# Optimization experiments

Measured on AMD Instinct MI355X. Metric: run time of the kernel, lower is better.

Reference implementation:

```python
import jax, jax.numpy as jnp
import numpy as np

NUM_QUERIES = 256
NUM_NEGATIVES = 512
NUM_GENERALIZED = 8
GEN_RADIUS = 1.0
TEMP = 0.5
STRONG_THRESHOLD = 0.97


def _mls(mu0, mu1, s0, s1):
    # mutual likelihood score; mu's are L2-normalized (F.normalize, eps=1e-12)
    mu0 = mu0 / jnp.maximum(jnp.linalg.norm(mu0, axis=-1, keepdims=True), 1e-12)
    mu1 = mu1 / jnp.maximum(jnp.linalg.norm(mu1, axis=-1, keepdims=True), 1e-12)
    down = s0 + s1
    return -0.5 * (((mu0 - mu1) ** 2) / down + jnp.log(down)).mean(-1)


def setup_inputs() -> dict:
    key = jax.random.key(0)
    B, S, H, W, C = 4, 19, 128, 128, 256
    ks = jax.random.split(key, 6)
    mu = jax.random.normal(ks[0], (B, C, H, W), jnp.float32)
    sigma = jax.random.uniform(ks[1], (B, C, H, W), jnp.float32, minval=0.1, maxval=1.0)
    cls = jax.random.randint(ks[2], (B, H, W), 0, S)
    label = jnp.transpose(jax.nn.one_hot(cls, S, dtype=jnp.float32), (0, 3, 1, 2))  # [B,S,H,W]
    mask = jnp.ones((B, 1, H, W), jnp.float32)
    prob = jax.random.uniform(ks[3], (B, S, H, W), jnp.float32)
    mmt_prototype_mu = jax.random.normal(ks[4], (S, 1, C), jnp.float32)
    mmt_prototype_sigma = jax.random.uniform(ks[5], (S, 1, C), jnp.float32, minval=0.1, maxval=1.0)
    return {"mu": mu, "sigma": sigma, "label": label, "mask": mask, "prob": prob,
            "mmt_prototype_mu": mmt_prototype_mu, "mmt_prototype_sigma": mmt_prototype_sigma,
            "epoch": 0, "iter_i": 0}


def reference(mu, sigma, label, mask, prob, mmt_prototype_mu, mmt_prototype_sigma, epoch, iter_i):
    B, C, H, W = mu.shape
    S = label.shape[1]
    P = B * H * W
    Q, NEG, G = NUM_QUERIES, NUM_NEGATIVES, NUM_GENERALIZED
    key = jax.random.key(1234)

    valid = (label * mask).transpose(1, 0, 2, 3).reshape(S, P)            # [S,P] float
    mu_f = mu.transpose(0, 2, 3, 1).reshape(P, C)                          # [P,C]
    sg_f = sigma.transpose(0, 2, 3, 1).reshape(P, C)
    prob_f = prob.transpose(1, 0, 2, 3).reshape(S, P)
    hard = (prob_f < STRONG_THRESHOLD).astype(valid.dtype) * valid         # [S,P]

    # --- segment prototypes (precision-weighted fusion), detached as in torch.no_grad ---
    inv_sg = 1.0 / sg_f
    proto_sigma_b = 1.0 / jnp.einsum('sp,pc->sc', valid, inv_sg)           # [S,C]
    proto_mu_b = proto_sigma_b * jnp.einsum('sp,pc->sc', valid, inv_sg * mu_f)
    mmt_mu = mmt_prototype_mu[:, 0, :]
    mmt_sg = mmt_prototype_sigma[:, 0, :]
    proto_sigma = 1.0 / (1.0 / proto_sigma_b + 1.0 / mmt_sg)               # momentum fusion
    proto_mu = proto_sigma * (mmt_mu / mmt_sg + proto_mu_b / proto_sigma_b)
    proto_mu = jax.lax.stop_gradient(proto_mu)
    proto_sigma = jax.lax.stop_gradient(proto_sigma)

    # cumulative masks for uniform sampling over valid / hard pixels via searchsorted
    valid_cum = jnp.cumsum(valid, axis=1)                                  # [S,P]
    valid_cnt = valid_cum[:, -1]
    hard_cum = jnp.cumsum(hard, axis=1)
    hard_cnt = hard_cum[:, -1]

    loss = jnp.float32(0.0)
    for i in range(S):
        ki = jax.random.fold_in(key, i)
        k_anc, k_cls, k_neg, k_gen = jax.random.split(ki, 4)
        # anchors: uniform over hard pixels of segment i
        u = jax.random.uniform(k_anc, (Q,)) * hard_cnt[i]
        a_idx = jnp.clip(jnp.searchsorted(hard_cum[i], u, side='right'), 0, P - 1)
        anchor_mu = mu_f[a_idx]                                            # [Q,C]
        anchor_sg = sg_f[a_idx]
        # negative class distribution from prototype MLS similarity
        others = jnp.concatenate([jnp.arange(i + 1, S), jnp.arange(0, i)])  # [S-1]
        sim = _mls(proto_mu[i][None], proto_mu[others], proto_sigma[i][None], proto_sigma[others])
        logp = jax.nn.log_softmax(sim / TEMP)
        samp = jax.random.categorical(k_cls, logp, shape=(Q, NEG))          # idx into `others`
        cls_g = others[samp.reshape(-1)]                                    # [Q*NEG] global class
        # uniform pixel within each sampled class (vectorized searchsorted over classes)
        un = jax.random.uniform(k_neg, (Q * NEG,))
        idx_all = jax.vmap(lambda cs, cnt: jnp.searchsorted(cs, un * cnt, side='right'))(valid_cum, valid_cnt)
        n_idx = jnp.clip(idx_all[cls_g, jnp.arange(Q * NEG)], 0, P - 1)
        neg_mu = jax.lax.stop_gradient(mu_f[n_idx].reshape(Q, NEG, C))
        neg_sg = jax.lax.stop_gradient(sg_f[n_idx].reshape(Q, NEG, C))
        pos_mu = jnp.broadcast_to(proto_mu[i][None, None], (Q, 1, C))
        pos_sg = jnp.broadcast_to(proto_sigma[i][None, None], (Q, 1, C))
        # generalized negatives: reparameterized samples from (updated) momentum prototypes
        eps = jax.random.normal(k_gen, (S - 1, G, C))
        gen = proto_mu[others][:, None, :] + GEN_RADIUS * jnp.sqrt(proto_sigma[others])[:, None, :] * eps
        gen = jnp.broadcast_to(gen.reshape(1, (S - 1) * G, C), (Q, (S - 1) * G, C))
        all_mu = jnp.concatenate([pos_mu, neg_mu, gen], axis=1)             # [Q,1+NEG+(S-1)*G,C]
        all_sg = jnp.concatenate([pos_sg, neg_sg, jnp.zeros_like(gen)], axis=1)
        logits = _mls(anchor_mu[:, None, :], all_mu, anchor_sg[:, None, :], all_sg) / TEMP
        loss = loss - jax.nn.log_softmax(logits, axis=-1)[:, 0].mean()      # CE vs target 0
    return loss / S
```

## Files before the change

kernel.cpp:

```cpp
#include <hip/hip_runtime.h>
#include <hip/hip_fp16.h>
#include <hip/hip_fp8.h>
#include <cstdint>

#define B_   4
#define S_   19
#define HW_  16384
#define P_   65536
#define C_   256
#define Q_   256
#define NEG_ 512
#define NS_  131072
#define GENV_ 144
#define NANCH (S_ * 256)
#define NPAIR (NANCH / 2)
#define NBUCK 8

typedef float v2f __attribute__((ext_vector_type(2)));

#if __has_builtin(__builtin_amdgcn_cvt_pk_f32_fp8) && __has_builtin(__builtin_amdgcn_cvt_pk_fp8_f32)
#define HAVE_HW_FP8 1
#endif

template<int W> __device__ __forceinline__ v2f cvt8(uint32_t d) {
#ifdef HAVE_HW_FP8
  v2f r = __builtin_amdgcn_cvt_pk_f32_fp8((int)d, W);
  return r;
#else
  __hip_fp8_e4m3 h0, h1;
  h0.__x = (uint8_t)(d >> (W * 16));
  h1.__x = (uint8_t)(d >> (W * 16 + 8));
  v2f r; r.x = (float)h0; r.y = (float)h1; return r;
#endif
}
template<int W> __device__ __forceinline__ uint32_t pk8(float a, float b, uint32_t old) {
#ifdef HAVE_HW_FP8
  return (uint32_t)__builtin_amdgcn_cvt_pk_fp8_f32(a, b, (int)old, W);
#else
  __hip_fp8_e4m3 ha(a), hb(b);
  uint32_t v = (uint32_t)ha.__x | ((uint32_t)hb.__x << 8);
  return (old & (W ? 0x0000FFFFu : 0xFFFF0000u)) | (v << (W * 16));
#endif
}

__device__ __forceinline__ void tf2x32(uint32_t k0, uint32_t k1, uint32_t x0, uint32_t x1,
                                       uint32_t& o0, uint32_t& o1) {
  uint32_t k2 = k0 ^ k1 ^ 0x1BD11BDAu;
#define TFR(r) { x0 += x1; x1 = (x1 << r) | (x1 >> (32 - r)); x1 ^= x0; }
  x0 += k0; x1 += k1;
  TFR(13) TFR(15) TFR(26) TFR(6)  x0 += k1; x1 += k2 + 1u;
  TFR(17) TFR(29) TFR(16) TFR(24) x0 += k2; x1 += k0 + 2u;
  TFR(13) TFR(15) TFR(26) TFR(6)  x0 += k0; x1 += k1 + 3u;
  TFR(17) TFR(29) TFR(16) TFR(24) x0 += k1; x1 += k2 + 4u;
  TFR(13) TFR(15) TFR(26) TFR(6)  x0 += k2; x1 += k0 + 5u;
#undef TFR
  o0 = x0; o1 = x1;
}

__device__ __forceinline__ uint32_t rbits(uint32_t k0, uint32_t k1, uint32_t n) {
  uint32_t a, b; tf2x32(k0, k1, 0u, n, a, b); return a ^ b;
}

__device__ __forceinline__ float bits2f01(uint32_t b) {
  return __uint_as_float((b >> 9) | 0x3f800000u) - 1.0f;
}

__device__ __forceinline__ float fastrcp(float x) {
  float r; asm("v_rcp_f32 %0, %1" : "=v"(r) : "v"(x)); return r;
}

__device__ __forceinline__ float wred(float v) {
#pragma unroll
  for (int off = 32; off > 0; off >>= 1) v += __shfl_xor(v, off, 64);
  return v;
}
__device__ __forceinline__ void wred3(float& a, float& b, float& c) {
#pragma unroll
  for (int off = 32; off > 0; off >>= 1) {
    a += __shfl_xor(a, off, 64);
    b += __shfl_xor(b, off, 64);
    c += __shfl_xor(c, off, 64);
  }
}

__device__ __forceinline__ void lse_up(float lg, float& m, float& l) {
  if (lg > m) { l = l * __expf(m - lg) + 1.0f; m = lg; }
  else l += __expf(lg - m);
}
__device__ __forceinline__ void lse_merge(float& m, float& l, float mo, float lo) {
  float mn = fmaxf(m, mo);
  l = l * __expf(m - mn) + lo * __expf(mo - mn);
  m = mn;
}

__device__ __forceinline__ float erfinv_f(float x) {
  float w = -__logf(fmaxf(fmaf(-x, x, 1.0f), 1e-37f));
  float p;
  if (w < 5.0f) {
    w -= 2.5f;
    p = 2.81022636e-08f;
    p = fmaf(p, w, 3.43273939e-07f);
    p = fmaf(p, w, -3.5233877e-06f);
    p = fmaf(p, w, -4.39150654e-06f);
    p = fmaf(p, w, 0.00021858087f);
    p = fmaf(p, w, -0.00125372503f);
    p = fmaf(p, w, -0.00417768164f);
    p = fmaf(p, w, 0.246640727f);
    p = fmaf(p, w, 1.50140941f);
  } else {
    w = sqrtf(w) - 3.0f;
    p = -0.000200214257f;
    p = fmaf(p, w, 0.000100950558f);
    p = fmaf(p, w, 0.00134934322f);
    p = fmaf(p, w, -0.00367342844f);
    p = fmaf(p, w, 0.00573950773f);
    p = fmaf(p, w, -0.0076224613f);
    p = fmaf(p, w, 0.00943887047f);
    p = fmaf(p, w, 1.00167406f);
    p = fmaf(p, w, 2.83297682f);
  }
  return p * x;
}

__global__ __launch_bounds__(256) void k_classify(const float* __restrict__ label,
    const float* __restrict__ mask, const float* __restrict__ prob,
    uint32_t* __restrict__ keys, int* __restrict__ cls, int* __restrict__ hrd,
    int* __restrict__ bcv, int* __restrict__ bch) {
  __shared__ int hv[S_], hh[S_];
  int t = threadIdx.x;
  if (t < S_) { hv[t] = 0; hh[t] = 0; }
  if (blockIdx.x == 0 && t < S_) {
    uint32_t f0, f1;
    tf2x32(0u, 1234u, 0u, (uint32_t)t, f0, f1);
#pragma unroll
    for (int k = 0; k < 4; ++k) {
      uint32_t a, b;
      tf2x32(f0, f1, 0u, (uint32_t)k, a, b);
      keys[t * 8 + k * 2] = a; keys[t * 8 + k * 2 + 1] = b;
    }
  }
  __syncthreads();
  int p = blockIdx.x * 256 + t;
  int b = p >> 14, rem = p & (HW_ - 1);
  int sp = -1;
#pragma unroll
  for (int s = 0; s < S_; ++s) {
    float l = label[((b * S_ + s) << 14) + rem];
    if (l > 0.5f) sp = s;
  }
  if (mask[(b << 14) + rem] <= 0.5f) sp = -1;
  int h = 0;
  if (sp >= 0) h = (prob[((b * S_ + sp) << 14) + rem] < 0.97f) ? 1 : 0;
  cls[p] = sp; hrd[p] = h;
  if (sp >= 0) { atomicAdd(&hv[sp], 1); if (h) atomicAdd(&hh[sp], 1); }
  __syncthreads();
  if (t < S_) { bcv[t * 256 + blockIdx.x] = hv[t]; bch[t * 256 + blockIdx.x] = hh[t]; }
}

__global__ __launch_bounds__(256) void k_norm(const float* __restrict__ mu,
    float2* __restrict__ rnrm) {
  int p = blockIdx.x * 256 + threadIdx.x;
  int b = p >> 14, rem = p & (HW_ - 1);
  const float* base = mu + (((size_t)(b * C_)) << 14) + rem;
  float s2 = 0.f;
#pragma unroll 4
  for (int c = 0; c < C_; ++c) {
    float v = base[(size_t)c << 14];
    s2 = fmaf(v, v, s2);
  }
  float nrm = sqrtf(s2);
  rnrm[p] = make_float2(fastrcp(fmaxf(nrm, 1e-12f)), nrm);
}

__global__ __launch_bounds__(256) void k_pack(const float* __restrict__ mu,
    const float* __restrict__ sg, const float2* __restrict__ rnrm,
    uint32_t* __restrict__ pair8) {
  __shared__ float smu[64][65];
  __shared__ float ssg[64][65];
  __shared__ float srn[64];
  int p0 = blockIdx.x * 64, c0 = blockIdx.y * 64;
  int b = p0 >> 14, rem0 = p0 & (HW_ - 1);
  if (threadIdx.x < 64) srn[threadIdx.x] = rnrm[p0 + threadIdx.x].x;
  int px = threadIdx.x & 63, cy = threadIdx.x >> 6;
#pragma unroll
  for (int itr = 0; itr < 16; ++itr) {
    int cl = cy + itr * 4;
    int addr = ((b * C_ + c0 + cl) << 14) + rem0 + px;
    smu[cl][px] = mu[addr];
    ssg[cl][px] = sg[addr];
  }
  __syncthreads();
#pragma unroll
  for (int itr = 0; itr < 8; ++itr) {
    int e = itr * 256 + threadIdx.x;
    int pxl = e >> 5, dw = e & 31, cl = dw * 2;
    float rn = srn[pxl];
    uint32_t wd = pk8<0>(smu[cl][pxl] * rn, ssg[cl][pxl], 0u);
    wd = pk8<1>(smu[cl + 1][pxl] * rn, ssg[cl + 1][pxl], wd);
    pair8[(size_t)(p0 + pxl) * 128 + (c0 >> 1) + dw] = wd;
  }
}

__global__ __launch_bounds__(320) void k_scan(const int* __restrict__ bcv, const int* __restrict__ bch,
    int* __restrict__ bov, int* __restrict__ boh,
    int* __restrict__ cntv, int* __restrict__ cnth,
    int* __restrict__ basev, int* __restrict__ baseh) {
  __shared__ int psv[S_][16], psh[S_][16], scv[S_], sch[S_];
  int t = threadIdx.x;
  int s = t >> 4, c = t & 15;
  if (t < 304) {
    int sv = 0, sh = 0;
#pragma unroll 4
    for (int b = 0; b < 16; ++b) {
      sv += bcv[s * 256 + c * 16 + b];
      sh += bch[s * 256 + c * 16 + b];
    }
    psv[s][c] = sv; psh[s][c] = sh;
  }
  __syncthreads();
  if (t < S_) {
    int rv = 0, rh = 0;
#pragma unroll
    for (int cc = 0; cc < 16; ++cc) {
      int tv = psv[t][cc]; psv[t][cc] = rv; rv += tv;
      int th = psh[t][cc]; psh[t][cc] = rh; rh += th;
    }
    cntv[t] = rv; cnth[t] = rh; scv[t] = rv; sch[t] = rh;
  }
  __syncthreads();
  if (t == 0) {
    int bv = 0, bh = 0;
    for (int k = 0; k < S_; ++k) { basev[k] = bv; bv += scv[k]; baseh[k] = bh; bh += sch[k]; }
  }
  if (t < 304) {
    int rv = psv[s][c], rh = psh[s][c];
#pragma unroll 4
    for (int b = 0; b < 16; ++b) {
      int i0 = s * 256 + c * 16 + b;
      int tv = bcv[i0]; bov[i0] = rv; rv += tv;
      int th = bch[i0]; boh[i0] = rh; rh += th;
    }
  }
}

__global__ __launch_bounds__(256) void k_fill(const int* __restrict__ cls, const int* __restrict__ hrd,
    const int* __restrict__ bov, const int* __restrict__ boh,
    const int* __restrict__ basev, const int* __restrict__ baseh,
    int* __restrict__ posv, int* __restrict__ posh) {
  __shared__ int lc[256], lh[256];
  int t = threadIdx.x;
  int p = blockIdx.x * 256 + t;
  int s = cls[p]; int h = hrd[p];
  lc[t] = s; lh[t] = h;
  __syncthreads();
  if (s >= 0) {
    int rv = 0, rh = 0;
    for (int k = 0; k < t; ++k) { if (lc[k] == s) { rv++; rh += lh[k]; } }
    posv[basev[s] + bov[s * 256 + blockIdx.x] + rv] = p;
    if (h) posh[baseh[s] + boh[s * 256 + blockIdx.x] + rh] = p;
  }
}

__global__ __launch_bounds__(256) void k_sums(const uint32_t* __restrict__ pair8,
    const float2* __restrict__ rnrm, const int* __restrict__ cls, float* __restrict__ part) {
  __shared__ float lacc[S_][2][C_];
  __shared__ int scls[256];
  __shared__ float snrm[256];
  int t = threadIdx.x;
  for (int e = t; e < S_ * 2 * C_; e += 256) (&lacc[0][0][0])[e] = 0.f;
  int p0 = blockIdx.x * 256;
  scls[t] = cls[p0 + t];
  snrm[t] = rnrm[p0 + t].y;
  __syncthreads();
  int half = t & 1, dwi = t >> 1;
  uint32_t d = pair8[(size_t)p0 * 128 + dwi];
  for (int pp = 0; pp < 256; ++pp) {
    uint32_t dnx = (pp + 1 < 256) ? pair8[(size_t)(p0 + pp + 1) * 128 + dwi] : 0u;
    int s = scls[pp];
    if (s >= 0) {
      v2f e = half ? cvt8<1>(d) : cvt8<0>(d);
      float ia = fastrcp(e.y);
      lacc[s][0][t] += ia;
      lacc[s][1][t] += ia * e.x * snrm[pp];
    }
    d = dnx;
  }
  __syncthreads();
  float* dst = part + (size_t)blockIdx.x * (2 * S_ * C_);
  for (int e = t; e < S_ * 2 * C_; e += 256) dst[e] = (&lacc[0][0][0])[e];
}

__global__ __launch_bounds__(256) void k_proto(const float* __restrict__ part,
    const float* __restrict__ mmu, const float* __restrict__ msg,
    float* __restrict__ pmu, float* __restrict__ psig, float* __restrict__ phat) {
  int s = blockIdx.x, c = threadIdx.x;
  float A = 0.f, Bv = 0.f;
  for (int b = 0; b < 256; ++b) {
    const float* pb = part + (size_t)b * (2 * S_ * C_) + (s * 2) * C_;
    A += pb[c];
    Bv += pb[C_ + c];
  }
  int e = s * C_ + c;
  float psb = 1.0f / A;
  float pmb = psb * Bv;
  float ms = msg[e], mm = mmu[e];
  float ps = 1.0f / (1.0f / psb + 1.0f / ms);
  float pm = ps * (mm / ms + pmb / psb);
  pmu[e] = pm; psig[e] = ps;
  __shared__ float red[4];
  float w = wred(pm * pm);
  int lane = c & 63, wv = c >> 6;
  if (lane == 0) red[wv] = w;
  __syncthreads();
  float tot = red[0] + red[1] + red[2] + red[3];
  float nrm = fmaxf(sqrtf(tot), 1e-12f);
  phat[e] = pm / nrm;
}

__global__ __launch_bounds__(64) void k_simlogp(const float* __restrict__ phat,
    const float* __restrict__ psig, float* __restrict__ logp) {
  int i = blockIdx.x, lane = threadIdx.x;
  int c0 = lane * 4;
  float phi[4], psi[4];
#pragma unroll
  for (int k = 0; k < 4; ++k) { phi[k] = phat[i * C_ + c0 + k]; psi[k] = psig[i * C_ + c0 + k]; }
  float xs[18];
#pragma unroll
  for (int j = 0; j < 18; ++j) {
    int o = i + 1 + j; if (o >= S_) o -= S_;
    float t = 0.f;
#pragma unroll
    for (int k = 0; k < 4; ++k) {
      float d = phi[k] - phat[o * C_ + c0 + k];
      float dn = psi[k] + psig[o * C_ + c0 + k];
      t += d * d / dn + logf(dn);
    }
    t = wred(t);
    xs[j] = (-0.5f * t * (1.0f / 256.0f)) * 2.0f;
  }
  float m = xs[0];
#pragma unroll
  for (int j = 1; j < 18; ++j) m = fmaxf(m, xs[j]);
  float se = 0.f;
#pragma unroll
  for (int j = 0; j < 18; ++j) se += expf(xs[j] - m);
  float lg = logf(se);
  if (lane == 0) {
#pragma unroll
    for (int j = 0; j < 18; ++j) logp[i * 18 + j] = xs[j] - m - lg;
  }
}

__global__ __launch_bounds__(256) void k_gen(const uint32_t* __restrict__ keys,
    const float* __restrict__ pmu, const float* __restrict__ psig, float* __restrict__ ghat) {
  int v = blockIdx.x, i = blockIdx.y, c = threadIdx.x;
  int o = i + 1 + (v >> 3); if (o >= S_) o -= S_;
  uint32_t k0 = keys[i * 8 + 6], k1 = keys[i * 8 + 7];
  uint32_t bits = rbits(k0, k1, (uint32_t)(v * C_ + c));
  float f01 = bits2f01(bits);
  const float lo = -0.99999994f;
  float u = fmaxf(f01 * 2.0f + lo, lo);
  float eps = 1.41421356237f * erfinv_f(u);
  float g = pmu[o * C_ + c] + sqrtf(psig[o * C_ + c]) * eps;
  __shared__ float red[4];
  float w = wred(g * g);
  int lane = c & 63, wv = c >> 6;
  if (lane == 0) red[wv] = w;
  __syncthreads();
  float tot = red[0] + red[1] + red[2] + red[3];
  float nrm = fmaxf(sqrtf(tot), 1e-12f);
  ghat[((size_t)(i * GENV_ + v)) * C_ + c] = g / nrm;
}

__global__ __launch_bounds__(256) void k_sample(const uint32_t* __restrict__ keys,
    const float* __restrict__ logp, const int* __restrict__ cntv, const int* __restrict__ basev,
    const int* __restrict__ posv, int* __restrict__ nidx) {
  int i = blockIdx.y;
  int m = blockIdx.x * 256 + threadIdx.x;
  __shared__ float elp[18];
  __shared__ int lcnt[S_], lbase[S_];
  int t = threadIdx.x;
  if (t < 18) elp[t] = __expf(-logp[i * 18 + t]);
  if (t < S_) { lcnt[t] = cntv[t]; lbase[t] = basev[t]; }
  __syncthreads();
  uint32_t kc0 = keys[i * 8 + 2], kc1 = keys[i * 8 + 3];
  uint32_t kn0 = keys[i * 8 + 4], kn1 = keys[i * 8 + 5];
  float bv = 1e30f; int best = 0;
  for (int s = 0; s < 18; ++s) {
    uint32_t b = rbits(kc0, kc1, (uint32_t)m * 18u + (uint32_t)s);
    float u = fmaxf(bits2f01(b), 1.17549435e-38f);
    float val = (-__logf(u)) * elp[s];
    if (val < bv) { bv = val; best = s; }
  }
  float un = bits2f01(rbits(kn0, kn1, (uint32_t)m));
  int cc = i + 1 + best; if (cc >= S_) cc -= S_;
  int cnt = lcnt[cc];
  int idx = P_ - 1;
  if (cnt > 0) {
    int kk = (int)(un * (float)cnt);
    if (kk >= cnt) kk = cnt - 1;
    idx = posv[lbase[cc] + kk];
  }
  nidx[(size_t)i * NS_ + m] = idx;
}

__global__ __launch_bounds__(64) void k_bucket(const uint32_t* __restrict__ keys,
    const int* __restrict__ cnth, const int* __restrict__ baseh, const int* __restrict__ posh,
    const int* __restrict__ nidx, int* __restrict__ snidx, int* __restrict__ boff,
    int* __restrict__ aidx) {
  int a = blockIdx.x;
  int lane = threadIdx.x;
  if (lane == 0) {
    int i = a >> 8, q = a & 255;
    uint32_t k0 = keys[i * 8 + 0], k1 = keys[i * 8 + 1];
    float u = bits2f01(rbits(k0, k1, (uint32_t)q));
    int cnt = cnth[i];
    int idx = P_ - 1;
    if (cnt > 0) {
      int kk = (int)(u * (float)cnt);
      if (kk >= cnt) kk = cnt - 1;
      idx = posh[baseh[i] + kk];
    }
    aidx[a] = idx;
  }
  const int* src = nidx + (size_t)a * NEG_;
  int e[8], bk[8];
#pragma unroll
  for (int c = 0; c < 8; ++c) { e[c] = src[c * 64 + lane]; bk[c] = (e[c] >> 13) & 7; }
  uint32_t cnt[NBUCK];
#pragma unroll
  for (int b = 0; b < NBUCK; ++b) cnt[b] = 0;
#pragma unroll
  for (int c = 0; c < 8; ++c)
#pragma unroll
    for (int b = 0; b < NBUCK; ++b) {
      unsigned long long mb = __ballot(bk[c] == b);
      cnt[b] += (uint32_t)__popcll(mb);
    }
  uint32_t base[NBUCK]; uint32_t run = 0;
#pragma unroll
  for (int b = 0; b < NBUCK; ++b) { base[b] = run; run += cnt[b]; }
  if (lane < NBUCK) boff[a * 9 + lane] = (int)base[lane];
  if (lane == 0) boff[a * 9 + 8] = NEG_;
  uint32_t off[NBUCK];
#pragma unroll
  for (int b = 0; b < NBUCK; ++b) off[b] = 0;
  unsigned long long ltm = (1ull << lane) - 1ull;
#pragma unroll
  for (int c = 0; c < 8; ++c) {
    int pos = 0;
#pragma unroll
    for (int b = 0; b < NBUCK; ++b) {
      unsigned long long mb = __ballot(bk[c] == b);
      if (bk[c] == b) pos = (int)(base[b] + off[b] + (uint32_t)__popcll(mb & ltm));
      off[b] += (uint32_t)__popcll(mb);
    }
    snidx[(size_t)a * NEG_ + pos] = e[c];
  }
}

__global__ __launch_bounds__(64) void k_neg(const uint32_t* __restrict__ pair8,
    const int* __restrict__ snidx, const int* __restrict__ boff,
    const int* __restrict__ aidx, float2* __restrict__ partial) {
  __shared__ float4 anc[260];
  int bid = blockIdx.x;
  int bucket = bid & 7;
  int pr = bid >> 3;
  int a0 = pr * 2, a1 = a0 + 1;
  int lane = threadIdx.x;

  int ap0 = aidx[a0], ap1 = aidx[a1];
  uint2 d0 = ((const uint2*)(pair8 + (size_t)ap0 * 128))[lane];
  uint2 d1 = ((const uint2*)(pair8 + (size_t)ap1 * 128))[lane];
  {
    v2f ex = cvt8<0>(d0.x), ey = cvt8<1>(d0.x), ez = cvt8<0>(d0.y), ew = cvt8<1>(d0.y);
    anc[lane * 2]     = make_float4(ex.x, ex.y, ey.x, ey.y);
    anc[lane * 2 + 1] = make_float4(ez.x, ez.y, ew.x, ew.y);
    ex = cvt8<0>(d1.x); ey = cvt8<1>(d1.x); ez = cvt8<0>(d1.y); ew = cvt8<1>(d1.y);
    anc[130 + lane * 2]     = make_float4(ex.x, ex.y, ey.x, ey.y);
    anc[130 + lane * 2 + 1] = make_float4(ez.x, ez.y, ew.x, ew.y);
  }
  __syncthreads();

  int s0 = boff[a0 * 9 + bucket], e0i = boff[a0 * 9 + bucket + 1];
  int s1 = boff[a1 * 9 + bucket], e1i = boff[a1 * 9 + bucket + 1];
  int L0 = e0i - s0, L1 = e1i - s1, Lt = L0 + L1;
  const int* list0 = snidx + (size_t)a0 * NEG_ + s0;
  const int* list1 = snidx + (size_t)a1 * NEG_ + s1;

  float m0 = -1e30f, l0 = 0.f, m1 = -1e30f, l1 = 0.f;

  for (int r = 0; r * 64 < Lt; ++r) {
    int g = r * 64 + lane;
    bool act = g < Lt;
    int which = (act && g >= L0) ? 1 : 0;
    int j = which ? (g - L0) : g;
    int p = act ? (which ? list1[j] : list0[j]) : ap0;
    const uint4* rp = (const uint4*)(pair8 + (size_t)p * 128);
    const float4* A = anc + which * 130;
    float sT = 0.f, sL = 0.f;
    uint4 c0 = rp[0], c1 = rp[1];
#pragma unroll 1
    for (int it = 0; it < 16; ++it) {
      int nx = ((it + 1) & 15) * 2;
      uint4 n0 = rp[nx], n1 = rp[nx + 1];
      uint32_t dws[8] = {c0.x, c0.y, c0.z, c0.w, c1.x, c1.y, c1.z, c1.w};
      float pp = 1.0f, pq = 1.0f;
#pragma unroll
      for (int gq = 0; gq < 4; ++gq) {
        float4 acA = A[it * 8 + gq * 2];
        float4 acB = A[it * 8 + gq * 2 + 1];
        v2f e0v = cvt8<0>(dws[2 * gq]),     e1v = cvt8<1>(dws[2 * gq]);
        v2f e2v = cvt8<0>(dws[2 * gq + 1]), e3v = cvt8<1>(dws[2 * gq + 1]);
        float dn0 = acA.y + e0v.y, dn1 = acA.w + e1v.y;
        float dn2 = acB.y + e2v.y, dn3 = acB.w + e3v.y;
        float d01 = dn0 * dn1, d23 = dn2 * dn3;
        float R01 = fastrcp(d01), R23 = fastrcp(d23);
        pp *= d01; pq *= d23;
        float r0 = dn1 * R01, r1 = dn0 * R01, r2 = dn3 * R23, r3 = dn2 * R23;
        float f0 = acA.x - e0v.x, f1 = acA.z - e1v.x;
        float f2 = acB.x - e2v.x, f3 = acB.z - e3v.x;
        sT = fmaf(f0 * f0, r0, sT); sT = fmaf(f1 * f1, r1, sT);
        sT = fmaf(f2 * f2, r2, sT); sT = fmaf(f3 * f3, r3, sT);
      }
      sL += __logf(pp * pq);
      c0 = n0; c1 = n1;
    }
    float lg = -(sT + sL) * (1.0f / 256.0f);
    if (act) { if (which) lse_up(lg, m1, l1); else lse_up(lg, m0, l0); }
  }
#pragma unroll
  for (int o = 32; o > 0; o >>= 1) {
    float mo = __shfl_xor(m0, o, 64), lo = __shfl_xor(l0, o, 64);
    lse_merge(m0, l0, mo, lo);
    mo = __shfl_xor(m1, o, 64); lo = __shfl_xor(l1, o, 64);
    lse_merge(m1, l1, mo, lo);
  }
  if (lane == 0) {
    partial[a0 * NBUCK + bucket] = make_float2(m0, l0);
    partial[a1 * NBUCK + bucket] = make_float2(m1, l1);
  }
}

__global__ __launch_bounds__(256, 4) void k_fin(const uint32_t* __restrict__ pair8,
    const float* __restrict__ phat, const float* __restrict__ psig,
    const float* __restrict__ ghat, const int* __restrict__ aidx,
    const float2* __restrict__ partial, float* __restrict__ out) {
  __shared__ float2 ancG[C_];
  __shared__ float redm[3][4];
  __shared__ float2 mlw[4];

  int bid = blockIdx.x;
  int i = bid >> 8;
  int t = threadIdx.x, w = t >> 6, lane = t & 63;

  int ap = aidx[bid];
  uint32_t ad = pair8[(size_t)ap * 128 + (t >> 1)];
  v2f ae0 = cvt8<0>(ad), ae1 = cvt8<1>(ad);
  float ahat = (t & 1) ? ae1.x : ae0.x;
  float asg = (t & 1) ? ae1.y : ae0.y;
  float wv = fastrcp(asg);
  ancG[t] = make_float2(wv, ahat * wv);

  float pm = phat[i * C_ + t];
  float ps = psig[i * C_ + t];
  float dnp = asg + ps;
  float dd = ahat - pm;
  float post = fmaf(dd * dd, fastrcp(dnp), __logf(dnp));
  float a1t = ahat * ahat * wv;
  float lat = __logf(asg);
  wred3(post, a1t, lat);
  if (lane == 0) { redm[0][w] = post; redm[1][w] = a1t; redm[2][w] = lat; }
  __syncthreads();
  float postS = redm[0][0] + redm[0][1] + redm[0][2] + redm[0][3];
  float Kc = (redm[1][0] + redm[1][1] + redm[1][2] + redm[1][3])
           + (redm[2][0] + redm[2][1] + redm[2][2] + redm[2][3]);
  float logit0 = -postS * (1.0f / 256.0f);

  float m = -1e30f, l = 0.0f;
  const float4* ancGf = (const float4*)ancG;
  if (lane < 36) {
    int g = lane * 4 + w;
    const float4* gp = (const float4*)(ghat + ((size_t)(i * GENV_ + g)) * C_);
    float a1 = 0.f, a2 = 0.f;
    for (int itr = 0; itr < 64; ++itr) {
      float4 gv = gp[itr];
      float4 g01 = ancGf[itr * 2];
      float4 g23 = ancGf[itr * 2 + 1];
      a1 = fmaf(gv.x * gv.x, g01.x, a1); a2 = fmaf(gv.x, g01.y, a2);
      a1 = fmaf(gv.y * gv.y, g01.z, a1); a2 = fmaf(gv.y, g01.w, a2);
      a1 = fmaf(gv.z * gv.z, g23.x, a1); a2 = fmaf(gv.z, g23.y, a2);
      a1 = fmaf(gv.w * gv.w, g23.z, a1); a2 = fmaf(gv.w, g23.w, a2);
    }
    float lg = -(Kc + a1 - 2.0f * a2) * (1.0f / 256.0f);
    lse_up(lg, m, l);
  }
#pragma unroll
  for (int o = 32; o > 0; o >>= 1) {
    float mo = __shfl_xor(m, o, 64);
    float lo = __shfl_xor(l, o, 64);
    lse_merge(m, l, mo, lo);
  }
  if (lane == 0) mlw[w] = make_float2(m, l);
  __syncthreads();
  if (t == 0) {
    float mm = mlw[0].x, ll = mlw[0].y;
    lse_merge(mm, ll, mlw[1].x, mlw[1].y);
    lse_merge(mm, ll, mlw[2].x, mlw[2].y);
    lse_merge(mm, ll, mlw[3].x, mlw[3].y);
    const float2* pp = partial + (size_t)bid * NBUCK;
#pragma unroll
    for (int b = 0; b < NBUCK; ++b) lse_merge(mm, ll, pp[b].x, pp[b].y);
    lse_merge(mm, ll, logit0, 1.0f);
    float lse = mm + __logf(ll);
    float contrib = logit0 - lse;
    atomicAdd(out, -contrib * (1.0f / (19.0f * 256.0f)));
  }
}

extern "C" void kernel_launch(void* const* d_in, const int* in_sizes, int n_in,
                              void* d_out, int out_size, void* d_ws, size_t ws_size,
                              hipStream_t stream) {
  const float* mu    = (const float*)d_in[0];
  const float* sg    = (const float*)d_in[1];
  const float* label = (const float*)d_in[2];
  const float* mask  = (const float*)d_in[3];
  const float* prob  = (const float*)d_in[4];
  const float* mmu   = (const float*)d_in[5];
  const float* msg   = (const float*)d_in[6];

  char* ws = (char*)d_ws;
  size_t off = 0;
  auto take = [&](size_t bytes) { size_t r = off; off = (off + bytes + 255) & ~(size_t)255; return r; };
  size_t o_pair8 = take((size_t)P_ * 128 * 4);
  size_t o_rnrm  = take((size_t)P_ * 8);
  size_t o_cls   = take((size_t)P_ * 4);
  size_t o_hrd   = take((size_t)P_ * 4);
  size_t o_bcv   = take(S_ * 256 * 4);
  size_t o_bch   = take(S_ * 256 * 4);
  size_t o_bov   = take(S_ * 256 * 4);
  size_t o_boh   = take(S_ * 256 * 4);
  size_t o_cntv  = take(S_ * 4);
  size_t o_cnth  = take(S_ * 4);
  size_t o_basev = take(S_ * 4);
  size_t o_baseh = take(S_ * 4);
  size_t o_posv  = take((size_t)P_ * 4);
  size_t o_posh  = take((size_t)P_ * 4);
  size_t o_part  = take((size_t)256 * 2 * S_ * C_ * 4);
  size_t o_pmu   = take(S_ * C_ * 4);
  size_t o_psig  = take(S_ * C_ * 4);
  size_t o_phat  = take(S_ * C_ * 4);
  size_t o_logp  = take(S_ * 18 * 4);
  size_t o_keys  = take(S_ * 8 * 4);
  size_t o_aidx  = take(S_ * Q_ * 4);
  size_t o_nidx  = take((size_t)S_ * NS_ * 4);
  size_t o_snidx = take((size_t)S_ * NS_ * 4);
  size_t o_boff  = take((size_t)NANCH * 9 * 4);
  size_t o_lpar  = take((size_t)NANCH * NBUCK * 8);
  size_t o_ghat  = take((size_t)S_ * GENV_ * C_ * 4);
  if (ws_size < off) return;

  uint32_t* pair8 = (uint32_t*)(ws + o_pair8);
  float2*   rnrm  = (float2*)(ws + o_rnrm);
  int*      cls   = (int*)(ws + o_cls);
  int*      hrd   = (int*)(ws + o_hrd);
  int*      bcv   = (int*)(ws + o_bcv);
  int*      bch   = (int*)(ws + o_bch);
  int*      bov   = (int*)(ws + o_bov);
  int*      boh   = (int*)(ws + o_boh);
  int*      cntv  = (int*)(ws + o_cntv);
  int*      cnth  = (int*)(ws + o_cnth);
  int*      basev = (int*)(ws + o_basev);
  int*      baseh = (int*)(ws + o_baseh);
  int*      posv  = (int*)(ws + o_posv);
  int*      posh  = (int*)(ws + o_posh);
  float*    part  = (float*)(ws + o_part);
  float*    pmu   = (float*)(ws + o_pmu);
  float*    psig  = (float*)(ws + o_psig);
  float*    phat  = (float*)(ws + o_phat);
  float*    logp  = (float*)(ws + o_logp);
  uint32_t* keys  = (uint32_t*)(ws + o_keys);
  int*      aidx  = (int*)(ws + o_aidx);
  int*      nidx  = (int*)(ws + o_nidx);
  int*      snidx = (int*)(ws + o_snidx);
  int*      boff  = (int*)(ws + o_boff);
  float2*   lpar  = (float2*)(ws + o_lpar);
  float*    ghat  = (float*)(ws + o_ghat);

  hipMemsetAsync(d_out, 0, (size_t)out_size * 4, stream);

  k_classify<<<256, 256, 0, stream>>>(label, mask, prob, keys, cls, hrd, bcv, bch);
  k_norm<<<256, 256, 0, stream>>>(mu, rnrm);
  k_pack<<<dim3(P_ / 64, C_ / 64), 256, 0, stream>>>(mu, sg, rnrm, pair8);
  k_scan<<<1, 320, 0, stream>>>(bcv, bch, bov, boh, cntv, cnth, basev, baseh);
  k_fill<<<256, 256, 0, stream>>>(cls, hrd, bov, boh, basev, baseh, posv, posh);
  k_sums<<<256, 256, 0, stream>>>(pair8, rnrm, cls, part);
  k_proto<<<S_, 256, 0, stream>>>(part, mmu, msg, pmu, psig, phat);
  k_simlogp<<<S_, 64, 0, stream>>>(phat, psig, logp);
  k_gen<<<dim3(GENV_, S_), 256, 0, stream>>>(keys, pmu, psig, ghat);
  k_sample<<<dim3(512, S_), 256, 0, stream>>>(keys, logp, cntv, basev, posv, nidx);
  k_bucket<<<NANCH, 64, 0, stream>>>(keys, cnth, baseh, posh, nidx, snidx, boff, aidx);
  k_neg<<<NBUCK * NPAIR, 64, 0, stream>>>(pair8, snidx, boff, aidx, lpar);
  k_fin<<<NANCH, 256, 0, stream>>>(pair8, phat, psig, ghat, aidx, lpar, (float*)d_out);
}
```

Measured before the change: 616.2 us.

## Merge small pipeline kernels to cut launches and parallelize proto reduction

```diff
diff --git a/kernel.cpp b/kernel.cpp
--- a/kernel.cpp
+++ b/kernel.cpp
@@ -124,8 +124,9 @@
 
 __global__ __launch_bounds__(256) void k_classify(const float* __restrict__ label,
     const float* __restrict__ mask, const float* __restrict__ prob,
+    const float* __restrict__ mu,
     uint32_t* __restrict__ keys, int* __restrict__ cls, int* __restrict__ hrd,
-    int* __restrict__ bcv, int* __restrict__ bch) {
+    int* __restrict__ bcv, int* __restrict__ bch, float2* __restrict__ rnrm) {
   __shared__ int hv[S_], hh[S_];
   int t = threadIdx.x;
   if (t < S_) { hv[t] = 0; hh[t] = 0; }
@@ -155,17 +156,11 @@
   if (sp >= 0) { atomicAdd(&hv[sp], 1); if (h) atomicAdd(&hh[sp], 1); }
   __syncthreads();
   if (t < S_) { bcv[t * 256 + blockIdx.x] = hv[t]; bch[t * 256 + blockIdx.x] = hh[t]; }
-}
-
-__global__ __launch_bounds__(256) void k_norm(const float* __restrict__ mu,
-    float2* __restrict__ rnrm) {
-  int p = blockIdx.x * 256 + threadIdx.x;
-  int b = p >> 14, rem = p & (HW_ - 1);
-  const float* base = mu + (((size_t)(b * C_)) << 14) + rem;
+  const float* basep = mu + (((size_t)(b * C_)) << 14) + rem;
   float s2 = 0.f;
-#pragma unroll 4
+#pragma unroll 8
   for (int c = 0; c < C_; ++c) {
-    float v = base[(size_t)c << 14];
+    float v = basep[(size_t)c << 14];
     s2 = fmaf(v, v, s2);
   }
   float nrm = sqrtf(s2);
@@ -243,45 +238,39 @@
   }
 }
 
-__global__ __launch_bounds__(256) void k_fill(const int* __restrict__ cls, const int* __restrict__ hrd,
+__global__ __launch_bounds__(256) void k_fillsums(const uint32_t* __restrict__ pair8,
+    const float2* __restrict__ rnrm, const int* __restrict__ cls, const int* __restrict__ hrd,
     const int* __restrict__ bov, const int* __restrict__ boh,
     const int* __restrict__ basev, const int* __restrict__ baseh,
-    int* __restrict__ posv, int* __restrict__ posh) {
-  __shared__ int lc[256], lh[256];
+    int* __restrict__ posv, int* __restrict__ posh, float* __restrict__ part) {
+  __shared__ float lacc[S_][2][C_];
+  __shared__ int scls[256];
+  __shared__ int slh[256];
+  __shared__ float snrm[256];
   int t = threadIdx.x;
-  int p = blockIdx.x * 256 + t;
+  int p0 = blockIdx.x * 256;
+  int p = p0 + t;
   int s = cls[p]; int h = hrd[p];
-  lc[t] = s; lh[t] = h;
+  scls[t] = s; slh[t] = h;
+  snrm[t] = rnrm[p].y;
+  for (int e = t; e < S_ * 2 * C_; e += 256) (&lacc[0][0][0])[e] = 0.f;
   __syncthreads();
   if (s >= 0) {
     int rv = 0, rh = 0;
-    for (int k = 0; k < t; ++k) { if (lc[k] == s) { rv++; rh += lh[k]; } }
+    for (int k = 0; k < t; ++k) { if (scls[k] == s) { rv++; rh += slh[k]; } }
     posv[basev[s] + bov[s * 256 + blockIdx.x] + rv] = p;
     if (h) posh[baseh[s] + boh[s * 256 + blockIdx.x] + rh] = p;
   }
-}
-
-__global__ __launch_bounds__(256) void k_sums(const uint32_t* __restrict__ pair8,
-    const float2* __restrict__ rnrm, const int* __restrict__ cls, float* __restrict__ part) {
-  __shared__ float lacc[S_][2][C_];
-  __shared__ int scls[256];
-  __shared__ float snrm[256];
-  int t = threadIdx.x;
-  for (int e = t; e < S_ * 2 * C_; e += 256) (&lacc[0][0][0])[e] = 0.f;
-  int p0 = blockIdx.x * 256;
-  scls[t] = cls[p0 + t];
-  snrm[t] = rnrm[p0 + t].y;
-  __syncthreads();
   int half = t & 1, dwi = t >> 1;
   uint32_t d = pair8[(size_t)p0 * 128 + dwi];
   for (int pp = 0; pp < 256; ++pp) {
     uint32_t dnx = (pp + 1 < 256) ? pair8[(size_t)(p0 + pp + 1) * 128 + dwi] : 0u;
-    int s = scls[pp];
-    if (s >= 0) {
+    int sc = scls[pp];
+    if (sc >= 0) {
       v2f e = half ? cvt8<1>(d) : cvt8<0>(d);
       float ia = fastrcp(e.y);
-      lacc[s][0][t] += ia;
-      lacc[s][1][t] += ia * e.x * snrm[pp];
+      lacc[sc][0][t] += ia;
+      lacc[sc][1][t] += ia * e.x * snrm[pp];
     }
     d = dnx;
   }
@@ -290,31 +279,44 @@
   for (int e = t; e < S_ * 2 * C_; e += 256) dst[e] = (&lacc[0][0][0])[e];
 }
 
-__global__ __launch_bounds__(256) void k_proto(const float* __restrict__ part,
+__global__ __launch_bounds__(1024) void k_proto(const float* __restrict__ part,
     const float* __restrict__ mmu, const float* __restrict__ msg,
     float* __restrict__ pmu, float* __restrict__ psig, float* __restrict__ phat) {
-  int s = blockIdx.x, c = threadIdx.x;
+  __shared__ float redA[4][C_];
+  __shared__ float redB[4][C_];
+  __shared__ float red[4];
+  int s = blockIdx.x;
+  int t = threadIdx.x;
+  int c = t & 255, grp = t >> 8;
   float A = 0.f, Bv = 0.f;
-  for (int b = 0; b < 256; ++b) {
+  for (int b = grp * 64; b < grp * 64 + 64; ++b) {
     const float* pb = part + (size_t)b * (2 * S_ * C_) + (s * 2) * C_;
     A += pb[c];
     Bv += pb[C_ + c];
   }
-  int e = s * C_ + c;
-  float psb = 1.0f / A;
-  float pmb = psb * Bv;
-  float ms = msg[e], mm = mmu[e];
-  float ps = 1.0f / (1.0f / psb + 1.0f / ms);
-  float pm = ps * (mm / ms + pmb / psb);
-  pmu[e] = pm; psig[e] = ps;
-  __shared__ float red[4];
-  float w = wred(pm * pm);
-  int lane = c & 63, wv = c >> 6;
-  if (lane == 0) red[wv] = w;
-  __syncthreads();
-  float tot = red[0] + red[1] + red[2] + red[3];
-  float nrm = fmaxf(sqrtf(tot), 1e-12f);
-  phat[e] = pm / nrm;
+  redA[grp][c] = A; redB[grp][c] = Bv;
+  __syncthreads();
+  float pm = 0.f;
+  if (grp == 0) {
+    A = redA[0][c] + redA[1][c] + redA[2][c] + redA[3][c];
+    Bv = redB[0][c] + redB[1][c] + redB[2][c] + redB[3][c];
+    int e = s * C_ + c;
+    float psb = 1.0f / A;
+    float pmb = psb * Bv;
+    float ms = msg[e], mm = mmu[e];
+    float ps = 1.0f / (1.0f / psb + 1.0f / ms);
+    pm = ps * (mm / ms + pmb / psb);
+    pmu[e] = pm; psig[e] = ps;
+    float w = wred(pm * pm);
+    int lane = c & 63, wv = c >> 6;
+    if (lane == 0) red[wv] = w;
+  }
+  __syncthreads();
+  if (grp == 0) {
+    float tot = red[0] + red[1] + red[2] + red[3];
+    float nrm = fmaxf(sqrtf(tot), 1e-12f);
+    phat[s * C_ + c] = pm / nrm;
+  }
 }
 
 __global__ __launch_bounds__(64) void k_simlogp(const float* __restrict__ phat,
@@ -351,57 +353,60 @@
   }
 }
 
-__global__ __launch_bounds__(256) void k_gen(const uint32_t* __restrict__ keys,
-    const float* __restrict__ pmu, const float* __restrict__ psig, float* __restrict__ ghat) {
-  int v = blockIdx.x, i = blockIdx.y, c = threadIdx.x;
-  int o = i + 1 + (v >> 3); if (o >= S_) o -= S_;
-  uint32_t k0 = keys[i * 8 + 6], k1 = keys[i * 8 + 7];
-  uint32_t bits = rbits(k0, k1, (uint32_t)(v * C_ + c));
-  float f01 = bits2f01(bits);
-  const float lo = -0.99999994f;
-  float u = fmaxf(f01 * 2.0f + lo, lo);
-  float eps = 1.41421356237f * erfinv_f(u);
-  float g = pmu[o * C_ + c] + sqrtf(psig[o * C_ + c]) * eps;
+__global__ __launch_bounds__(256) void k_gensample(const uint32_t* __restrict__ keys,
+    const float* __restrict__ pmu, const float* __restrict__ psig,
+    const float* __restrict__ logp, const int* __restrict__ cntv, const int* __restrict__ basev,
+    const int* __restrict__ posv, float* __restrict__ ghat, int* __restrict__ nidx) {
   __shared__ float red[4];
-  float w = wred(g * g);
-  int lane = c & 63, wv = c >> 6;
-  if (lane == 0) red[wv] = w;
-  __syncthreads();
-  float tot = red[0] + red[1] + red[2] + red[3];
-  float nrm = fmaxf(sqrtf(tot), 1e-12f);
-  ghat[((size_t)(i * GENV_ + v)) * C_ + c] = g / nrm;
-}
-
-__global__ __launch_bounds__(256) void k_sample(const uint32_t* __restrict__ keys,
-    const float* __restrict__ logp, const int* __restrict__ cntv, const int* __restrict__ basev,
-    const int* __restrict__ posv, int* __restrict__ nidx) {
-  int i = blockIdx.y;
-  int m = blockIdx.x * 256 + threadIdx.x;
   __shared__ float elp[18];
   __shared__ int lcnt[S_], lbase[S_];
+  int bid = blockIdx.x;
   int t = threadIdx.x;
-  if (t < 18) elp[t] = __expf(-logp[i * 18 + t]);
-  if (t < S_) { lcnt[t] = cntv[t]; lbase[t] = basev[t]; }
-  __syncthreads();
-  uint32_t kc0 = keys[i * 8 + 2], kc1 = keys[i * 8 + 3];
-  uint32_t kn0 = keys[i * 8 + 4], kn1 = keys[i * 8 + 5];
-  float bv = 1e30f; int best = 0;
-  for (int s = 0; s < 18; ++s) {
-    uint32_t b = rbits(kc0, kc1, (uint32_t)m * 18u + (uint32_t)s);
-    float u = fmaxf(bits2f01(b), 1.17549435e-38f);
-    float val = (-__logf(u)) * elp[s];
-    if (val < bv) { bv = val; best = s; }
-  }
-  float un = bits2f01(rbits(kn0, kn1, (uint32_t)m));
-  int cc = i + 1 + best; if (cc >= S_) cc -= S_;
-  int cnt = lcnt[cc];
-  int idx = P_ - 1;
-  if (cnt > 0) {
-    int kk = (int)(un * (float)cnt);
-    if (kk >= cnt) kk = cnt - 1;
-    idx = posv[lbase[cc] + kk];
-  }
-  nidx[(size_t)i * NS_ + m] = idx;
+  if (bid < GENV_ * S_) {
+    int v = bid % GENV_, i = bid / GENV_;
+    int c = t;
+    int o = i + 1 + (v >> 3); if (o >= S_) o -= S_;
+    uint32_t k0 = keys[i * 8 + 6], k1 = keys[i * 8 + 7];
+    uint32_t bits = rbits(k0, k1, (uint32_t)(v * C_ + c));
+    float f01 = bits2f01(bits);
+    const float lo = -0.99999994f;
+    float u = fmaxf(f01 * 2.0f + lo, lo);
+    float eps = 1.41421356237f * erfinv_f(u);
+    float g = pmu[o * C_ + c] + sqrtf(psig[o * C_ + c]) * eps;
+    float w = wred(g * g);
+    int lane = c & 63, wv = c >> 6;
+    if (lane == 0) red[wv] = w;
+    __syncthreads();
+    float tot = red[0] + red[1] + red[2] + red[3];
+    float nrm = fmaxf(sqrtf(tot), 1e-12f);
+    ghat[((size_t)(i * GENV_ + v)) * C_ + c] = g / nrm;
+  } else {
+    int sid = bid - GENV_ * S_;
+    int i = sid / 512;
+    int m = (sid % 512) * 256 + t;
+    if (t < 18) elp[t] = __expf(-logp[i * 18 + t]);
+    if (t < S_) { lcnt[t] = cntv[t]; lbase[t] = basev[t]; }
+    __syncthreads();
+    uint32_t kc0 = keys[i * 8 + 2], kc1 = keys[i * 8 + 3];
+    uint32_t kn0 = keys[i * 8 + 4], kn1 = keys[i * 8 + 5];
+    float bv = 1e30f; int best = 0;
+    for (int s = 0; s < 18; ++s) {
+      uint32_t b = rbits(kc0, kc1, (uint32_t)m * 18u + (uint32_t)s);
+      float u = fmaxf(bits2f01(b), 1.17549435e-38f);
+      float val = (-__logf(u)) * elp[s];
+      if (val < bv) { bv = val; best = s; }
+    }
+    float un = bits2f01(rbits(kn0, kn1, (uint32_t)m));
+    int cc = i + 1 + best; if (cc >= S_) cc -= S_;
+    int cnt = lcnt[cc];
+    int idx = P_ - 1;
+    if (cnt > 0) {
+      int kk = (int)(un * (float)cnt);
+      if (kk >= cnt) kk = cnt - 1;
+      idx = posv[lbase[cc] + kk];
+    }
+    nidx[(size_t)i * NS_ + m] = idx;
+  }
 }
 
 __global__ __launch_bounds__(64) void k_bucket(const uint32_t* __restrict__ keys,
@@ -689,16 +694,13 @@
 
   hipMemsetAsync(d_out, 0, (size_t)out_size * 4, stream);
 
-  k_classify<<<256, 256, 0, stream>>>(label, mask, prob, keys, cls, hrd, bcv, bch);
-  k_norm<<<256, 256, 0, stream>>>(mu, rnrm);
+  k_classify<<<256, 256, 0, stream>>>(label, mask, prob, mu, keys, cls, hrd, bcv, bch, rnrm);
   k_pack<<<dim3(P_ / 64, C_ / 64), 256, 0, stream>>>(mu, sg, rnrm, pair8);
   k_scan<<<1, 320, 0, stream>>>(bcv, bch, bov, boh, cntv, cnth, basev, baseh);
-  k_fill<<<256, 256, 0, stream>>>(cls, hrd, bov, boh, basev, baseh, posv, posh);
-  k_sums<<<256, 256, 0, stream>>>(pair8, rnrm, cls, part);
-  k_proto<<<S_, 256, 0, stream>>>(part, mmu, msg, pmu, psig, phat);
+  k_fillsums<<<256, 256, 0, stream>>>(pair8, rnrm, cls, hrd, bov, boh, basev, baseh, posv, posh, part);
+  k_proto<<<S_, 1024, 0, stream>>>(part, mmu, msg, pmu, psig, phat);
   k_simlogp<<<S_, 64, 0, stream>>>(phat, psig, logp);
-  k_gen<<<dim3(GENV_, S_), 256, 0, stream>>>(keys, pmu, psig, ghat);
-  k_sample<<<dim3(512, S_), 256, 0, stream>>>(keys, logp, cntv, basev, posv, nidx);
+  k_gensample<<<GENV_ * S_ + 512 * S_, 256, 0, stream>>>(keys, pmu, psig, logp, cntv, basev, posv, ghat, nidx);
   k_bucket<<<NANCH, 64, 0, stream>>>(keys, cnth, baseh, posh, nidx, snidx, boff, aidx);
   k_neg<<<NBUCK * NPAIR, 64, 0, stream>>>(pair8, snidx, boff, aidx, lpar);
   k_fin<<<NANCH, 256, 0, stream>>>(pair8, phat, psig, ghat, aidx, lpar, (float*)d_out);
```

Result: no change. 604.1 us (-2.0%).
